# Optimization experiments

Measured on AMD Instinct MI355X. Metric: run time of the kernel, lower is better.

The kernel has to match this reference:

```python
import jax, jax.numpy as jnp
import numpy as np

FEATS = [(100, 100), (50, 50), (25, 25), (13, 13)]  # (W, H) per level
BS, NQ, D = 2, 10000, 256
NH, NL, NP, G = 8, 4, 4, 8
HD = D // NH


def grid_sample_bilinear(im, grid):
    """torch.nn.functional.grid_sample(mode='bilinear', padding_mode='zeros', align_corners=False).
    im: [N, C, H, W]; grid: [N, Hg, Wg, 2] in [-1, 1] (x, y). Returns [N, C, Hg, Wg]."""
    N, C, H, W = im.shape
    Hg, Wg = grid.shape[1], grid.shape[2]
    x = (grid[..., 0] + 1.0) * (W * 0.5) - 0.5
    y = (grid[..., 1] + 1.0) * (H * 0.5) - 0.5
    x0 = jnp.floor(x); y0 = jnp.floor(y)
    wx1 = x - x0; wx0 = 1.0 - wx1
    wy1 = y - y0; wy0 = 1.0 - wy1
    imf = im.reshape(N, C, H * W)

    def corner(xi, yi, w):
        inb = (xi >= 0) & (xi < W) & (yi >= 0) & (yi < H)
        xi_c = jnp.clip(xi, 0, W - 1).astype(jnp.int32)
        yi_c = jnp.clip(yi, 0, H - 1).astype(jnp.int32)
        idx = (yi_c * W + xi_c).reshape(N, 1, Hg * Wg)
        vals = jnp.take_along_axis(imf, idx, axis=2).reshape(N, C, Hg, Wg)
        return vals * (w * inb.astype(im.dtype))[:, None]

    out = (corner(x0, y0, wx0 * wy0) + corner(x0 + 1, y0, wx1 * wy0)
           + corner(x0, y0 + 1, wx0 * wy1) + corner(x0 + 1, y0 + 1, wx1 * wy1))
    return out


def setup_inputs() -> dict:
    key = jax.random.key(0)
    ks = jax.random.split(key, 7)
    nv = sum(w * h for (w, h) in FEATS)
    return {
        "query": jax.random.normal(ks[0], (BS, NQ, D), jnp.float32),
        "value": jax.random.normal(ks[1], (BS, nv, NH, HD), jnp.float32),
        "reference_points": jax.random.uniform(ks[2], (BS, NQ, NL, 2), jnp.float32),
        "spatial_shapes": jnp.array(FEATS, jnp.float32),  # rows are (W, H)
        "W_off": jax.random.normal(ks[3], (NH * NL * NP * 2, D), jnp.float32) * 0.02,
        "b_off": jax.random.normal(ks[4], (NH * NL * NP * 2,), jnp.float32) * 0.5,
        "W_attn": jax.random.normal(ks[5], (NH * NL * NP, D), jnp.float32) * 0.02,
        "b_attn": jax.random.normal(ks[6], (NH * NL * NP,), jnp.float32) * 0.02,
    }


def reference(query, value, reference_points, spatial_shapes, W_off, b_off, W_attn, b_attn):
    bs, nq, _ = query.shape
    # sampling offsets: [bs, nq, NH, NL*NP*2] with (level, point, xy) layout
    off = (jnp.einsum('bqd,od->bqo', query, W_off) + b_off).reshape(bs, nq, NH, NL * NP * 2)
    # reference points tiled to the same (level, point, xy) layout
    ref = jnp.broadcast_to(reference_points[:, :, None, :, None, :],
                           (bs, nq, NH, NL, NP, 2)).reshape(bs, nq, NH, NL * NP * 2)
    # offset normalizer: (1/W, 1/H) per level, tiled over points
    inv = 1.0 / spatial_shapes  # [NL, 2]
    norm = jnp.broadcast_to(inv[:, None, :], (NL, NP, 2)).reshape(-1)
    loc = (ref + off * norm) * 2.0 - 1.0  # [bs, nq, NH, NL*NP*2]
    loc = loc.reshape(bs, nq, NH, NL, NP, 2)

    # attention weights: softmax over (NL*NP), then rearranged to [bs*NH, 1, nq/G, NL*G*NP]
    aw = jax.nn.softmax((jnp.einsum('bqd,od->bqo', query, W_attn) + b_attn)
                        .reshape(bs, nq, NH, NL * NP), axis=-1)
    aw = aw.reshape(bs, nq // G, G, NH, NL, NP).transpose(0, 3, 1, 4, 2, 5)
    aw = aw.reshape(bs * NH, 1, nq // G, NL * G * NP)

    # per-level grid_sample
    sizes = [w * h for (w, h) in FEATS]
    starts = np.concatenate([[0], np.cumsum(sizes)]).tolist()
    sampled = []
    for lvl, (Wl, Hl) in enumerate(FEATS):
        val_l = value[:, starts[lvl]:starts[lvl + 1]]  # [bs, Hl*Wl, NH, HD]
        val_l = val_l.transpose(0, 2, 3, 1).reshape(bs * NH, HD, Hl, Wl)
        grid_l = loc[:, :, :, lvl].transpose(0, 2, 1, 3, 4)  # [bs, NH, nq, NP, 2]
        grid_l = grid_l.reshape(bs * NH, nq // G, G * NP, 2)
        sampled.append(grid_sample_bilinear(val_l, grid_l))  # [bs*NH, HD, nq/G, G*NP]
    sv = jnp.concatenate(sampled, axis=-1)  # [bs*NH, HD, nq/G, NL*G*NP]

    out = sv * aw
    # reduce_sum linear (fixed 0/1 weight from init_weights) == sum over levels and points per group slot
    out = out.reshape(bs * NH, HD, nq // G, NL, G, NP).sum(axis=(3, 5))  # [bs*NH, HD, nq/G, G]
    return out.reshape(bs, NH * HD, nq)
```

## Files before the change

kernel.cpp:

```cpp
#include <hip/hip_runtime.h>

#define NQ   10000
#define BSZ  2
#define DIM  256
#define NH   8
#define HD   32
#define NLV  4
#define NPT  4
#define NV   13294
#define MT   (BSZ*NQ)
#define NOUT 384
#define NVAL (BSZ*NV*NH*HD)
#define GEMM_BLOCKS 939
#define PREP_BLOCKS 6647

typedef float    floatx4 __attribute__((ext_vector_type(4)));
typedef int      intx4   __attribute__((ext_vector_type(4)));
typedef __bf16   bf16x8  __attribute__((ext_vector_type(8)));
typedef _Float16 halfx8  __attribute__((ext_vector_type(8)));
typedef _Float16 halfx4  __attribute__((ext_vector_type(4)));

__device__ __forceinline__ unsigned short f32_to_bf16(float f) {
  unsigned int u = __float_as_uint(f);
  u += 0x7FFFu + ((u >> 16) & 1u);
  return (unsigned short)(u >> 16);
}

__global__ __launch_bounds__(256) void gp_kernel(
    const float* __restrict__ query, const float* __restrict__ W_off,
    const float* __restrict__ W_attn,
    const float* __restrict__ b_off, const float* __restrict__ b_attn,
    const float* __restrict__ value,
    float* __restrict__ raw, _Float16* __restrict__ vf16) {
  const int bid = blockIdx.x;
  const int tid = threadIdx.x;
  if (bid >= GEMM_BLOCKS) {
    int i = (bid - GEMM_BLOCKS) * 256 + tid;
    if (i * 4 < NVAL) {
      floatx4 v = *(const floatx4*)&value[i * 4];
      halfx4 t = { (_Float16)v.x, (_Float16)v.y, (_Float16)v.z, (_Float16)v.w };
      *(uint2*)&vf16[i * 4] = *(const uint2*)&t;
    }
    return;
  }
  __shared__ unsigned short As[64][40];
  __shared__ unsigned short Bs[128][40];
  const int n0 = (bid % 3) * 128;
  const int m0 = (bid / 3) * 64;
  const int wave = tid >> 6;
  const int lane = tid & 63;
  const int quad = lane >> 4;
  const int l16  = lane & 15;
  floatx4 acc[8] = {};
  const int ar = tid >> 2;
  const int ac = (tid & 3) * 8;
  const int br = tid >> 1;
  const int bc = (tid & 1) * 16;
  const float* __restrict__ Wsrc =
      (n0 < 256) ? (W_off + (size_t)n0 * DIM) : (W_attn + (size_t)(n0 - 256) * DIM);

  for (int k0 = 0; k0 < DIM; k0 += 32) {
    {
      int gm = m0 + ar;
      floatx4 a0 = {}, a1 = {};
      if (gm < MT) {
        const float* src = query + (size_t)gm * DIM + k0 + ac;
        a0 = *(const floatx4*)src;
        a1 = *(const floatx4*)(src + 4);
      }
      unsigned short t[8];
      t[0]=f32_to_bf16(a0.x); t[1]=f32_to_bf16(a0.y); t[2]=f32_to_bf16(a0.z); t[3]=f32_to_bf16(a0.w);
      t[4]=f32_to_bf16(a1.x); t[5]=f32_to_bf16(a1.y); t[6]=f32_to_bf16(a1.z); t[7]=f32_to_bf16(a1.w);
      *(uint4*)&As[ar][ac] = *(const uint4*)t;
    }
    {
      const float* src = Wsrc + (size_t)br * DIM + k0 + bc;
      floatx4 b0 = *(const floatx4*)src;
      floatx4 b1 = *(const floatx4*)(src + 4);
      floatx4 b2 = *(const floatx4*)(src + 8);
      floatx4 b3 = *(const floatx4*)(src + 12);
      unsigned short t[16];
      t[0]=f32_to_bf16(b0.x);  t[1]=f32_to_bf16(b0.y);  t[2]=f32_to_bf16(b0.z);  t[3]=f32_to_bf16(b0.w);
      t[4]=f32_to_bf16(b1.x);  t[5]=f32_to_bf16(b1.y);  t[6]=f32_to_bf16(b1.z);  t[7]=f32_to_bf16(b1.w);
      t[8]=f32_to_bf16(b2.x);  t[9]=f32_to_bf16(b2.y);  t[10]=f32_to_bf16(b2.z); t[11]=f32_to_bf16(b2.w);
      t[12]=f32_to_bf16(b3.x); t[13]=f32_to_bf16(b3.y); t[14]=f32_to_bf16(b3.z); t[15]=f32_to_bf16(b3.w);
      *(uint4*)&Bs[br][bc]     = *(const uint4*)t;
      *(uint4*)&Bs[br][bc + 8] = *(const uint4*)(t + 8);
    }
    __syncthreads();
    bf16x8 a = *(const bf16x8*)&As[wave*16 + l16][quad*8];
    #pragma unroll
    for (int nt = 0; nt < 8; nt++) {
      bf16x8 b = *(const bf16x8*)&Bs[nt*16 + l16][quad*8];
      acc[nt] = __builtin_amdgcn_mfma_f32_16x16x32_bf16(a, b, acc[nt], 0, 0, 0);
    }
    __syncthreads();
  }
  #pragma unroll
  for (int nt = 0; nt < 8; nt++) {
    int gn = n0 + nt*16 + l16;
    float bias = (gn < 256) ? b_off[gn] : b_attn[gn - 256];
    #pragma unroll
    for (int r = 0; r < 4; r++) {
      int gm = m0 + wave*16 + quad*4 + r;
      if (gm < MT) raw[(size_t)gm*NOUT + gn] = acc[nt][r] + bias;
    }
  }
}

__global__ __launch_bounds__(256) void sample_kernel(
    const float* __restrict__ raw, const _Float16* __restrict__ vf16,
    const float* __restrict__ refp, float* __restrict__ tmp) {
  const int b  = blockIdx.y;
  const int q0 = blockIdx.x * 8;
  const int mbase = b * NQ + q0;
  const int tid = threadIdx.x;

  __shared__ int          s_off[64 * 68];
  __shared__ unsigned int s_w  [64 * 34];
  __shared__ float        s_aw [64 * 17];

  const int WLI[4] = {100, 50, 25, 13};
  const int STI[4] = {0, 10000, 12500, 13125};

  float rpx[4], rpy[4];

  #pragma unroll
  for (int it = 0; it < 4; ++it) {
    int slot = it * 256 + tid;
    int ql = slot >> 7, r = slot & 127, h = r >> 4, lp = r & 15, l = lp >> 2, p = lp & 3;
    int m = mbase + ql;
    const float* rp = raw + (size_t)m * NOUT;
    float offx = rp[h*32 + l*8 + p*2 + 0];
    float offy = rp[h*32 + l*8 + p*2 + 1];
    s_aw[(ql*8 + h)*17 + lp] = rp[256 + h*16 + lp];
    float Wl = (float)WLI[l];
    float rx = refp[(m*NLV + l)*2 + 0];
    float ry = refp[(m*NLV + l)*2 + 1];
    rpx[it] = rx * Wl + offx - 0.5f;
    rpy[it] = ry * Wl + offy - 0.5f;
  }
  __syncthreads();

  if (tid < 64) {
    int base = tid * 17;
    float mx = -1e30f;
    #pragma unroll
    for (int i = 0; i < 16; i++) mx = fmaxf(mx, s_aw[base + i]);
    float s = 0.f;
    float e[16];
    #pragma unroll
    for (int i = 0; i < 16; i++) { e[i] = expf(s_aw[base + i] - mx); s += e[i]; }
    float inv = 1.f / s;
    #pragma unroll
    for (int i = 0; i < 16; i++) s_aw[base + i] = e[i] * inv;
  }
  __syncthreads();

  #pragma unroll
  for (int it = 0; it < 4; ++it) {
    int slot = it * 256 + tid;
    int ql = slot >> 7, r = slot & 127, h = r >> 4, lp = r & 15, l = lp >> 2;
    int rowqh = ql*8 + h;
    float aw = s_aw[rowqh*17 + lp];
    float px = rpx[it], py = rpy[it];
    float x0f = floorf(px), y0f = floorf(py);
    int x0 = (int)x0f, y0 = (int)y0f;
    float wx1 = px - x0f, wx0 = 1.f - wx1;
    float wy1 = py - y0f, wy0 = 1.f - wy1;
    int Wl = WLI[l], STl = STI[l];
    int offs[4]; halfx4 wb;
    #pragma unroll
    for (int t = 0; t < 4; ++t) {
      int xi = x0 + (t & 1), yi = y0 + (t >> 1);
      bool inb = (xi >= 0) & (xi < Wl) & (yi >= 0) & (yi < Wl);
      offs[t] = inb ? ((STl + yi*Wl + xi) * 512 + h * 64) : 0;
      float w = inb ? (aw * ((t & 1) ? wx1 : wx0) * ((t >> 1) ? wy1 : wy0)) : 0.f;
      wb[t] = (_Float16)w;
    }
    *(intx4*)&s_off[rowqh*68 + lp*4] = *(const intx4*)offs;
    *(uint2*)&s_w[rowqh*34 + lp*2] = *(const uint2*)&wb;
  }
  __syncthreads();

  const int wv = tid >> 6, lane = tid & 63;
  const int qh = lane >> 5, ql = wv*2 + qh;
  const int h = (lane >> 2) & 7, cq = lane & 3;
  const char* vb = (const char*)vf16 + (size_t)b * (NV*NH*HD*2) + cq * 16;
  floatx4 acc0 = {0.f,0.f,0.f,0.f}, acc1 = {0.f,0.f,0.f,0.f};
  const int orow = (ql*8 + h) * 68, wrow = (ql*8 + h) * 34;
  #pragma unroll 4
  for (int pt = 0; pt < 16; ++pt) {
    intx4 offs = *(const intx4*)&s_off[orow + pt*4];
    uint2 wp   = *(const uint2*)&s_w[wrow + pt*2];
    halfx4 hw  = *(const halfx4*)&wp;
    halfx8 v0 = *(const halfx8*)(vb + offs.x);
    halfx8 v1 = *(const halfx8*)(vb + offs.y);
    halfx8 v2 = *(const halfx8*)(vb + offs.z);
    halfx8 v3 = *(const halfx8*)(vb + offs.w);
    #pragma unroll
    for (int t = 0; t < 4; ++t) {
      halfx8 v = (t==0) ? v0 : (t==1) ? v1 : (t==2) ? v2 : v3;
      float w = (float)hw[t];
      acc0.x += w * (float)v[0];
      acc0.y += w * (float)v[1];
      acc0.z += w * (float)v[2];
      acc0.w += w * (float)v[3];
      acc1.x += w * (float)v[4];
      acc1.y += w * (float)v[5];
      acc1.z += w * (float)v[6];
      acc1.w += w * (float)v[7];
    }
  }
  int m = mbase + ql;
  float* dst = &tmp[(size_t)m * DIM + h*HD + cq*8];
  *(floatx4*)dst       = acc0;
  *(floatx4*)(dst + 4) = acc1;
}

__global__ __launch_bounds__(256) void transpose_kernel(
    const float* __restrict__ tmp, float* __restrict__ out) {
  __shared__ float tile[32][33];
  const int b  = blockIdx.z;
  const int q0 = blockIdx.x * 32;
  const int c0 = blockIdx.y * 32;
  const int tx = threadIdx.x & 31;
  const int ty = threadIdx.x >> 5;
  #pragma unroll
  for (int i = 0; i < 4; i++) {
    int qq = q0 + ty + i*8;
    tile[ty + i*8][tx] = (qq < NQ) ? tmp[((long)b*NQ + qq)*DIM + c0 + tx] : 0.f;
  }
  __syncthreads();
  if (q0 + tx < NQ) {
    #pragma unroll
    for (int i = 0; i < 4; i++) {
      out[((long)b*DIM + c0 + ty + i*8)*NQ + q0 + tx] = tile[tx][ty + i*8];
    }
  }
}

extern "C" void kernel_launch(void* const* d_in, const int* in_sizes, int n_in,
                              void* d_out, int out_size, void* d_ws, size_t ws_size,
                              hipStream_t stream) {
  const float* query  = (const float*)d_in[0];
  const float* value  = (const float*)d_in[1];
  const float* refp   = (const float*)d_in[2];
  const float* W_off  = (const float*)d_in[4];
  const float* b_off  = (const float*)d_in[5];
  const float* W_attn = (const float*)d_in[6];
  const float* b_attn = (const float*)d_in[7];
  float* out = (float*)d_out;

  char* ws = (char*)d_ws;
  float*     raw  = (float*)ws;
  float*     tmp  = (float*)(ws + 30720000);
  _Float16*  vf16 = (_Float16*)(ws + 51200000);

  hipLaunchKernelGGL(gp_kernel, dim3(GEMM_BLOCKS + PREP_BLOCKS), dim3(256), 0, stream,
                     query, W_off, W_attn, b_off, b_attn, value, raw, vf16);
  hipLaunchKernelGGL(sample_kernel, dim3(NQ / 8, BSZ), dim3(256), 0, stream,
                     raw, vf16, refp, tmp);
  hipLaunchKernelGGL(transpose_kernel, dim3(313, 8, 2), dim3(256), 0, stream,
                     tmp, out);
}
```

Before: 170.6 us.

## Store intermediates in fp16 and drop LDS staging in projection GEMM

The projection GEMM now loads query and weight fragments straight from global memory into MFMA operands, with a cheaper packed bf16 conversion, and no longer stages them through shared memory with barriers. The GEMM output (offsets and attention logits) and the sampled per-query result are stored as fp16 rather than fp32, halving the intermediate traffic between the three kernels. The aim is to cut memory bandwidth and synchronisation cost. The trade-offs are lower precision for the sampling offsets, which are in pixel units up to about 100 where fp16 spacing is coarse, and for the outputs. The GEMM also loses operand reuse through LDS, so weight rows are re-read by every wave.

```diff
diff --git a/kernel.cpp b/kernel.cpp
--- a/kernel.cpp
+++ b/kernel.cpp
@@ -19,11 +19,16 @@
 typedef __bf16   bf16x8  __attribute__((ext_vector_type(8)));
 typedef _Float16 halfx8  __attribute__((ext_vector_type(8)));
 typedef _Float16 halfx4  __attribute__((ext_vector_type(4)));
-
-__device__ __forceinline__ unsigned short f32_to_bf16(float f) {
-  unsigned int u = __float_as_uint(f);
-  u += 0x7FFFu + ((u >> 16) & 1u);
-  return (unsigned short)(u >> 16);
+typedef _Float16 halfx2  __attribute__((ext_vector_type(2)));
+
+__device__ __forceinline__ unsigned pk_bf16(float lo, float hi) {
+  return __builtin_amdgcn_perm(__float_as_uint(hi) + 0x8000u,
+                               __float_as_uint(lo) + 0x8000u, 0x07060302);
+}
+
+__device__ __forceinline__ unsigned short f32_to_f16_bits(float f) {
+  _Float16 h = (_Float16)f;
+  return __builtin_bit_cast(unsigned short, h);
 }
 
 __global__ __launch_bounds__(256) void gp_kernel(
@@ -31,7 +36,7 @@
     const float* __restrict__ W_attn,
     const float* __restrict__ b_off, const float* __restrict__ b_attn,
     const float* __restrict__ value,
-    float* __restrict__ raw, _Float16* __restrict__ vf16) {
+    _Float16* __restrict__ rawh, _Float16* __restrict__ vf16) {
   const int bid = blockIdx.x;
   const int tid = threadIdx.x;
   if (bid >= GEMM_BLOCKS) {
@@ -43,58 +48,38 @@
     }
     return;
   }
-  __shared__ unsigned short As[64][40];
-  __shared__ unsigned short Bs[128][40];
   const int n0 = (bid % 3) * 128;
   const int m0 = (bid / 3) * 64;
   const int wave = tid >> 6;
   const int lane = tid & 63;
   const int quad = lane >> 4;
   const int l16  = lane & 15;
-  floatx4 acc[8] = {};
-  const int ar = tid >> 2;
-  const int ac = (tid & 3) * 8;
-  const int br = tid >> 1;
-  const int bc = (tid & 1) * 16;
+  const int mrow = m0 + wave*16 + l16;
+  const bool mok = mrow < MT;
+  const float* __restrict__ arow = query + (size_t)mrow * DIM;
   const float* __restrict__ Wsrc =
       (n0 < 256) ? (W_off + (size_t)n0 * DIM) : (W_attn + (size_t)(n0 - 256) * DIM);
-
+  const float* __restrict__ brow = Wsrc + (size_t)l16 * DIM;
+
+  floatx4 acc[8] = {};
+  #pragma unroll 2
   for (int k0 = 0; k0 < DIM; k0 += 32) {
-    {
-      int gm = m0 + ar;
-      floatx4 a0 = {}, a1 = {};
-      if (gm < MT) {
-        const float* src = query + (size_t)gm * DIM + k0 + ac;
-        a0 = *(const floatx4*)src;
-        a1 = *(const floatx4*)(src + 4);
-      }
-      unsigned short t[8];
-      t[0]=f32_to_bf16(a0.x); t[1]=f32_to_bf16(a0.y); t[2]=f32_to_bf16(a0.z); t[3]=f32_to_bf16(a0.w);
-      t[4]=f32_to_bf16(a1.x); t[5]=f32_to_bf16(a1.y); t[6]=f32_to_bf16(a1.z); t[7]=f32_to_bf16(a1.w);
-      *(uint4*)&As[ar][ac] = *(const uint4*)t;
-    }
-    {
-      const float* src = Wsrc + (size_t)br * DIM + k0 + bc;
-      floatx4 b0 = *(const floatx4*)src;
-      floatx4 b1 = *(const floatx4*)(src + 4);
-      floatx4 b2 = *(const floatx4*)(src + 8);
-      floatx4 b3 = *(const floatx4*)(src + 12);
-      unsigned short t[16];
-      t[0]=f32_to_bf16(b0.x);  t[1]=f32_to_bf16(b0.y);  t[2]=f32_to_bf16(b0.z);  t[3]=f32_to_bf16(b0.w);
-      t[4]=f32_to_bf16(b1.x);  t[5]=f32_to_bf16(b1.y);  t[6]=f32_to_bf16(b1.z);  t[7]=f32_to_bf16(b1.w);
-      t[8]=f32_to_bf16(b2.x);  t[9]=f32_to_bf16(b2.y);  t[10]=f32_to_bf16(b2.z); t[11]=f32_to_bf16(b2.w);
-      t[12]=f32_to_bf16(b3.x); t[13]=f32_to_bf16(b3.y); t[14]=f32_to_bf16(b3.z); t[15]=f32_to_bf16(b3.w);
-      *(uint4*)&Bs[br][bc]     = *(const uint4*)t;
-      *(uint4*)&Bs[br][bc + 8] = *(const uint4*)(t + 8);
-    }
-    __syncthreads();
-    bf16x8 a = *(const bf16x8*)&As[wave*16 + l16][quad*8];
+    const int k = k0 + quad*8;
+    floatx4 a0 = {}, a1 = {};
+    if (mok) { a0 = *(const floatx4*)(arow + k); a1 = *(const floatx4*)(arow + k + 4); }
+    uint4 ua = { pk_bf16(a0.x, a0.y), pk_bf16(a0.z, a0.w),
+                 pk_bf16(a1.x, a1.y), pk_bf16(a1.z, a1.w) };
+    bf16x8 a = __builtin_bit_cast(bf16x8, ua);
     #pragma unroll
     for (int nt = 0; nt < 8; nt++) {
-      bf16x8 b = *(const bf16x8*)&Bs[nt*16 + l16][quad*8];
-      acc[nt] = __builtin_amdgcn_mfma_f32_16x16x32_bf16(a, b, acc[nt], 0, 0, 0);
-    }
-    __syncthreads();
+      const float* bp = brow + nt*16*DIM + k;
+      floatx4 b0 = *(const floatx4*)bp;
+      floatx4 b1 = *(const floatx4*)(bp + 4);
+      uint4 ub = { pk_bf16(b0.x, b0.y), pk_bf16(b0.z, b0.w),
+                   pk_bf16(b1.x, b1.y), pk_bf16(b1.z, b1.w) };
+      acc[nt] = __builtin_amdgcn_mfma_f32_16x16x32_bf16(
+                    a, __builtin_bit_cast(bf16x8, ub), acc[nt], 0, 0, 0);
+    }
   }
   #pragma unroll
   for (int nt = 0; nt < 8; nt++) {
@@ -103,14 +88,14 @@
     #pragma unroll
     for (int r = 0; r < 4; r++) {
       int gm = m0 + wave*16 + quad*4 + r;
-      if (gm < MT) raw[(size_t)gm*NOUT + gn] = acc[nt][r] + bias;
+      if (gm < MT) rawh[(size_t)gm*NOUT + gn] = (_Float16)(acc[nt][r] + bias);
     }
   }
 }
 
 __global__ __launch_bounds__(256) void sample_kernel(
-    const float* __restrict__ raw, const _Float16* __restrict__ vf16,
-    const float* __restrict__ refp, float* __restrict__ tmp) {
+    const _Float16* __restrict__ rawh, const _Float16* __restrict__ vf16,
+    const float* __restrict__ refp, _Float16* __restrict__ tmph) {
   const int b  = blockIdx.y;
   const int q0 = blockIdx.x * 8;
   const int mbase = b * NQ + q0;
@@ -130,10 +115,10 @@
     int slot = it * 256 + tid;
     int ql = slot >> 7, r = slot & 127, h = r >> 4, lp = r & 15, l = lp >> 2, p = lp & 3;
     int m = mbase + ql;
-    const float* rp = raw + (size_t)m * NOUT;
-    float offx = rp[h*32 + l*8 + p*2 + 0];
-    float offy = rp[h*32 + l*8 + p*2 + 1];
-    s_aw[(ql*8 + h)*17 + lp] = rp[256 + h*16 + lp];
+    const _Float16* rp = rawh + (size_t)m * NOUT;
+    float offx = (float)rp[h*32 + l*8 + p*2 + 0];
+    float offy = (float)rp[h*32 + l*8 + p*2 + 1];
+    s_aw[(ql*8 + h)*17 + lp] = (float)rp[256 + h*16 + lp];
     float Wl = (float)WLI[l];
     float rx = refp[(m*NLV + l)*2 + 0];
     float ry = refp[(m*NLV + l)*2 + 1];
@@ -169,17 +154,19 @@
     float wx1 = px - x0f, wx0 = 1.f - wx1;
     float wy1 = py - y0f, wy0 = 1.f - wy1;
     int Wl = WLI[l], STl = STI[l];
-    int offs[4]; halfx4 wb;
+    int offs[4]; unsigned short wb[4];
     #pragma unroll
     for (int t = 0; t < 4; ++t) {
       int xi = x0 + (t & 1), yi = y0 + (t >> 1);
       bool inb = (xi >= 0) & (xi < Wl) & (yi >= 0) & (yi < Wl);
       offs[t] = inb ? ((STl + yi*Wl + xi) * 512 + h * 64) : 0;
       float w = inb ? (aw * ((t & 1) ? wx1 : wx0) * ((t >> 1) ? wy1 : wy0)) : 0.f;
-      wb[t] = (_Float16)w;
+      wb[t] = f32_to_f16_bits(w);
     }
     *(intx4*)&s_off[rowqh*68 + lp*4] = *(const intx4*)offs;
-    *(uint2*)&s_w[rowqh*34 + lp*2] = *(const uint2*)&wb;
+    uint2 wp = { (unsigned)wb[0] | ((unsigned)wb[1] << 16),
+                 (unsigned)wb[2] | ((unsigned)wb[3] << 16) };
+    *(uint2*)&s_w[rowqh*34 + lp*2] = wp;
   }
   __syncthreads();
 
@@ -193,7 +180,7 @@
   for (int pt = 0; pt < 16; ++pt) {
     intx4 offs = *(const intx4*)&s_off[orow + pt*4];
     uint2 wp   = *(const uint2*)&s_w[wrow + pt*2];
-    halfx4 hw  = *(const halfx4*)&wp;
+    halfx4 hw  = __builtin_bit_cast(halfx4, wp);
     halfx8 v0 = *(const halfx8*)(vb + offs.x);
     halfx8 v1 = *(const halfx8*)(vb + offs.y);
     halfx8 v2 = *(const halfx8*)(vb + offs.z);
@@ -213,13 +200,15 @@
     }
   }
   int m = mbase + ql;
-  float* dst = &tmp[(size_t)m * DIM + h*HD + cq*8];
-  *(floatx4*)dst       = acc0;
-  *(floatx4*)(dst + 4) = acc1;
+  uint4 st = { __builtin_bit_cast(unsigned, __builtin_amdgcn_cvt_pkrtz(acc0.x, acc0.y)),
+               __builtin_bit_cast(unsigned, __builtin_amdgcn_cvt_pkrtz(acc0.z, acc0.w)),
+               __builtin_bit_cast(unsigned, __builtin_amdgcn_cvt_pkrtz(acc1.x, acc1.y)),
+               __builtin_bit_cast(unsigned, __builtin_amdgcn_cvt_pkrtz(acc1.z, acc1.w)) };
+  *(uint4*)&tmph[(size_t)m * DIM + h*HD + cq*8] = st;
 }
 
 __global__ __launch_bounds__(256) void transpose_kernel(
-    const float* __restrict__ tmp, float* __restrict__ out) {
+    const _Float16* __restrict__ tmph, float* __restrict__ out) {
   __shared__ float tile[32][33];
   const int b  = blockIdx.z;
   const int q0 = blockIdx.x * 32;
@@ -229,13 +218,13 @@
   #pragma unroll
   for (int i = 0; i < 4; i++) {
     int qq = q0 + ty + i*8;
-    tile[ty + i*8][tx] = (qq < NQ) ? tmp[((long)b*NQ + qq)*DIM + c0 + tx] : 0.f;
+    tile[ty + i*8][tx] = (qq < NQ) ? (float)tmph[((size_t)b*NQ + qq)*DIM + c0 + tx] : 0.f;
   }
   __syncthreads();
   if (q0 + tx < NQ) {
     #pragma unroll
     for (int i = 0; i < 4; i++) {
-      out[((long)b*DIM + c0 + ty + i*8)*NQ + q0 + tx] = tile[tx][ty + i*8];
+      out[((size_t)b*DIM + c0 + ty + i*8)*NQ + q0 + tx] = tile[tx][ty + i*8];
     }
   }
 }
@@ -253,14 +242,14 @@
   float* out = (float*)d_out;
 
   char* ws = (char*)d_ws;
-  float*     raw  = (float*)ws;
-  float*     tmp  = (float*)(ws + 30720000);
-  _Float16*  vf16 = (_Float16*)(ws + 51200000);
+  _Float16* rawh = (_Float16*)ws;
+  _Float16* tmph = (_Float16*)(ws + 15360000);
+  _Float16* vf16 = (_Float16*)(ws + 25600000);
 
   hipLaunchKernelGGL(gp_kernel, dim3(GEMM_BLOCKS + PREP_BLOCKS), dim3(256), 0, stream,
-                     query, W_off, W_attn, b_off, b_attn, value, raw, vf16);
+                     query, W_off, W_attn, b_off, b_attn, value, rawh, vf16);
   hipLaunchKernelGGL(sample_kernel, dim3(NQ / 8, BSZ), dim3(256), 0, stream,
-                     raw, vf16, refp, tmp);
+                     rawh, vf16, refp, tmph);
   hipLaunchKernelGGL(transpose_kernel, dim3(313, 8, 2), dim3(256), 0, stream,
-                     tmp, out);
-}
+                     tmph, out);
+}
```

Measured after the change: 210.6 us. +23.4%, slower.
